# Kernel tuning notes

Measured on AMD Instinct MI355X. Metric: run time of the kernel, lower is better.

## Reference

```python
import jax, jax.numpy as jnp
import numpy as np

B, S, D, H = 4, 2048, 1024, 16
DK = D // H


def setup_inputs() -> dict:
    key = jax.random.key(0)
    ks = jax.random.split(key, 10)
    s = 0.02  # keep linear outputs well-scaled
    causal = jnp.triu(jnp.ones((S, S), dtype=bool), k=1)  # True = masked
    return {
        "Q": jax.random.normal(ks[0], (B, S, D), dtype=jnp.float32),
        "K_V": jax.random.normal(ks[1], (B, S, D), dtype=jnp.float32),
        "mask": jnp.broadcast_to(causal, (B, S, S)),
        "Wq": jax.random.normal(ks[2], (D, D), dtype=jnp.float32) * s,
        "bq": jnp.zeros((D,), dtype=jnp.float32),
        "Wk": jax.random.normal(ks[3], (D, D), dtype=jnp.float32) * s,
        "bk": jnp.zeros((D,), dtype=jnp.float32),
        "Wv": jax.random.normal(ks[4], (D, D), dtype=jnp.float32) * s,
        "bv": jnp.zeros((D,), dtype=jnp.float32),
        "Wo": jax.random.normal(ks[5], (D, D), dtype=jnp.float32) * s,
        "bo": jnp.zeros((D,), dtype=jnp.float32),
    }


def reference(Q, K_V, mask, Wq, bq, Wk, bk, Wv, bv, Wo, bo):
    # Linear projections
    q = Q @ Wq + bq          # [B, Sq, D]
    k = K_V @ Wk + bk        # [B, Sk, D]
    v = K_V @ Wv + bv        # [B, Sk, D]
    Sq, Sk = q.shape[1], k.shape[1]
    # chunk(dim=2)+cat(dim=0) == split into H heads of size DK
    q = q.reshape(B, Sq, H, DK)
    k = k.reshape(B, Sk, H, DK)
    v = v.reshape(B, Sk, H, DK)
    scale = 1.0 / jnp.sqrt(jnp.float32(DK))
    scores = jnp.einsum("bqhd,bkhd->bhqk", q, k) * scale  # [B,H,Sq,Sk]
    # mask.repeat(head_num,1,1) == broadcast mask over heads
    scores = jnp.where(mask[:, None, :, :], -jnp.inf, scores)
    attn = jax.nn.softmax(scores, axis=-1)
    # dropout is identity in eval mode
    out = jnp.einsum("bhqk,bkhd->bqhd", attn, v).reshape(B, Sq, D)
    return out @ Wo + bo
```

## Files before the change

### kernel.cpp

```cpp
#include <hip/hip_runtime.h>

typedef unsigned short u16;
typedef __attribute__((ext_vector_type(8))) __bf16 bf16x8;
typedef __attribute__((ext_vector_type(4))) float f32x4;

#define B_  4
#define S_  2048
#define D_  1024
#define H_  16
#define DK_ 64

__device__ __forceinline__ u16 f2bf(float f) {
  unsigned u = __float_as_uint(f);
  u += 0x7fffu + ((u >> 16) & 1u);
  return (u16)(u >> 16);
}
__device__ __forceinline__ u16 f2bf_trunc(float f) {
  return (u16)(__float_as_uint(f) >> 16);
}
__device__ __forceinline__ float hexp2(float f) {
  return __builtin_amdgcn_exp2f(f);
}

__device__ __forceinline__ void load_lds16(const u16* g, u16* l) {
  __builtin_amdgcn_global_load_lds((const __attribute__((address_space(1))) void*)g,
                                   (__attribute__((address_space(3))) void*)l,
                                   16, 0, 0);
}

__global__ void cvt_bf16_2(const float* __restrict__ x0, u16* __restrict__ y0,
                           const float* __restrict__ x1, u16* __restrict__ y1, int n4) {
  int i = blockIdx.x * blockDim.x + threadIdx.x;
  const float* x = x0; u16* y = y0;
  int j = i;
  if (i >= n4) { x = x1; y = y1; j = i - n4; }
  float4 v = ((const float4*)x)[j];
  ushort4 o;
  o.x = f2bf(v.x); o.y = f2bf(v.y); o.z = f2bf(v.z); o.w = f2bf(v.w);
  ((ushort4*)y)[j] = o;
}

__global__ void transpose_cvt4(const float* __restrict__ W0, const float* __restrict__ W1,
                               const float* __restrict__ W2, const float* __restrict__ W3,
                               u16* __restrict__ T0, u16* __restrict__ T1,
                               u16* __restrict__ T2, u16* __restrict__ T3) {
  __shared__ float tile[32][33];
  const float* W = (blockIdx.z == 0) ? W0 : (blockIdx.z == 1) ? W1 : (blockIdx.z == 2) ? W2 : W3;
  u16*         T = (blockIdx.z == 0) ? T0 : (blockIdx.z == 1) ? T1 : (blockIdx.z == 2) ? T2 : T3;
  int bx = blockIdx.x * 32, by = blockIdx.y * 32;
  int tx = threadIdx.x, ty = threadIdx.y;
  #pragma unroll
  for (int i = 0; i < 32; i += 8)
    tile[ty + i][tx] = W[(size_t)(by + ty + i) * D_ + bx + tx];
  __syncthreads();
  #pragma unroll
  for (int i = 0; i < 32; i += 8)
    T[(size_t)(bx + ty + i) * D_ + by + tx] = f2bf(tile[tx][ty + i]);
}

#define BM 128
#define BN 128
#define BK 32

__global__ __launch_bounds__(256, 2)
void gemm_qkv(const u16* __restrict__ Aq, const u16* __restrict__ Ak,
              const u16* __restrict__ Bt3,
              const float* __restrict__ bq, const float* __restrict__ bk,
              const float* __restrict__ bv,
              u16* __restrict__ qp, u16* __restrict__ kp, u16* __restrict__ vpT,
              float qscale) {
  __shared__ u16 As[BM * BK];
  __shared__ u16 Bs[BN * BK];
  const int tid  = threadIdx.x;
  const int lane = tid & 63, wave = tid >> 6;
  const int bm = blockIdx.x * BM;
  const int bn = blockIdx.y * BN;
  const int path = bn >> 10;
  const u16* A = (path == 0) ? Aq : Ak;
  const int wm = (wave >> 1) * 64, wn = (wave & 1) * 64;
  const int fm = lane & 15, fk4 = lane >> 4;
  const int K = D_;

  f32x4 acc[4][4] = {};

  const int r = tid >> 2;
  const int c = (tid & 3) * 8;
  const u16* gA0 = A   + (size_t)(bm + r) * K + c;
  const u16* gA1 = A   + (size_t)(bm + r + 64) * K + c;
  const u16* gB0 = Bt3 + (size_t)(bn + r) * K + c;
  const u16* gB1 = Bt3 + (size_t)(bn + r + 64) * K + c;
  u16* lA0 = &As[tid * 8];
  u16* lA1 = &As[2048 + tid * 8];
  u16* lB0 = &Bs[tid * 8];
  u16* lB1 = &Bs[2048 + tid * 8];

  for (int kt = 0; kt < K; kt += BK) {
    load_lds16(gA0 + kt, lA0);
    load_lds16(gA1 + kt, lA1);
    load_lds16(gB0 + kt, lB0);
    load_lds16(gB1 + kt, lB1);
    __syncthreads();
    bf16x8 af[4], bfr[4];
    #pragma unroll
    for (int i = 0; i < 4; ++i)
      af[i] = *(const bf16x8*)&As[(wm + i * 16 + fm) * BK + fk4 * 8];
    #pragma unroll
    for (int i = 0; i < 4; ++i)
      bfr[i] = *(const bf16x8*)&Bs[(wn + i * 16 + fm) * BK + fk4 * 8];
    #pragma unroll
    for (int i = 0; i < 4; ++i)
      #pragma unroll
      for (int j = 0; j < 4; ++j)
        acc[i][j] = __builtin_amdgcn_mfma_f32_16x16x32_bf16(af[i], bfr[j], acc[i][j], 0, 0, 0);
    __syncthreads();
  }

  #pragma unroll
  for (int i = 0; i < 4; ++i) {
    #pragma unroll
    for (int j = 0; j < 4; ++j) {
      int colg = bn + wn + j * 16 + fm;
      int rowg0 = bm + wm + i * 16 + fk4 * 4;
      if (path == 0) {
        float bb = bq[colg];
        #pragma unroll
        for (int rg = 0; rg < 4; ++rg)
          qp[(size_t)(rowg0 + rg) * D_ + colg] = f2bf((acc[i][j][rg] + bb) * qscale);
      } else if (path == 1) {
        int ck = colg - 1024;
        float bb = bk[ck];
        #pragma unroll
        for (int rg = 0; rg < 4; ++rg)
          kp[(size_t)(rowg0 + rg) * D_ + ck] = f2bf(acc[i][j][rg] + bb);
      } else {
        int cv = colg - 2048;
        float bb = bv[cv];
        int hh = cv >> 6, dk = cv & 63;
        int bbt = rowg0 >> 11, s = rowg0 & (S_ - 1);
        ushort4 pk4;
        pk4.x = f2bf(acc[i][j][0] + bb);
        pk4.y = f2bf(acc[i][j][1] + bb);
        pk4.z = f2bf(acc[i][j][2] + bb);
        pk4.w = f2bf(acc[i][j][3] + bb);
        *(ushort4*)&vpT[(((size_t)bbt * H_ + hh) * DK_ + dk) * S_ + s] = pk4;
      }
    }
  }
}

__global__ __launch_bounds__(256, 2)
void gemm_out(const u16* __restrict__ A, const u16* __restrict__ Bt,
              const float* __restrict__ bias, float* __restrict__ Cf) {
  __shared__ u16 As[BM * BK];
  __shared__ u16 Bs[BN * BK];
  const int tid  = threadIdx.x;
  const int lane = tid & 63, wave = tid >> 6;
  const int bm = blockIdx.x * BM;
  const int bn = blockIdx.y * BN;
  const int wm = (wave >> 1) * 64, wn = (wave & 1) * 64;
  const int fm = lane & 15, fk4 = lane >> 4;
  const int K = D_;

  f32x4 acc[4][4] = {};
  const int r = tid >> 2;
  const int c = (tid & 3) * 8;
  const u16* gA0 = A  + (size_t)(bm + r) * K + c;
  const u16* gA1 = A  + (size_t)(bm + r + 64) * K + c;
  const u16* gB0 = Bt + (size_t)(bn + r) * K + c;
  const u16* gB1 = Bt + (size_t)(bn + r + 64) * K + c;
  u16* lA0 = &As[tid * 8];
  u16* lA1 = &As[2048 + tid * 8];
  u16* lB0 = &Bs[tid * 8];
  u16* lB1 = &Bs[2048 + tid * 8];

  for (int kt = 0; kt < K; kt += BK) {
    load_lds16(gA0 + kt, lA0);
    load_lds16(gA1 + kt, lA1);
    load_lds16(gB0 + kt, lB0);
    load_lds16(gB1 + kt, lB1);
    __syncthreads();
    bf16x8 af[4], bfr[4];
    #pragma unroll
    for (int i = 0; i < 4; ++i)
      af[i] = *(const bf16x8*)&As[(wm + i * 16 + fm) * BK + fk4 * 8];
    #pragma unroll
    for (int i = 0; i < 4; ++i)
      bfr[i] = *(const bf16x8*)&Bs[(wn + i * 16 + fm) * BK + fk4 * 8];
    #pragma unroll
    for (int i = 0; i < 4; ++i)
      #pragma unroll
      for (int j = 0; j < 4; ++j)
        acc[i][j] = __builtin_amdgcn_mfma_f32_16x16x32_bf16(af[i], bfr[j], acc[i][j], 0, 0, 0);
    __syncthreads();
  }

  #pragma unroll
  for (int i = 0; i < 4; ++i)
    #pragma unroll
    for (int j = 0; j < 4; ++j) {
      int colg = bn + wn + j * 16 + fm;
      float bb = bias[colg];
      #pragma unroll
      for (int rg = 0; rg < 4; ++rg) {
        int rowg = bm + wm + i * 16 + fk4 * 4 + rg;
        Cf[(size_t)rowg * D_ + colg] = acc[i][j][rg] + bb;
      }
    }
}

#define PST 136

__global__ __launch_bounds__(256, 2)
void attn_kernel(const u16* __restrict__ qp, const u16* __restrict__ kp,
                 const u16* __restrict__ vpT, u16* __restrict__ ao) {
  __shared__ u16 Ks[16 * 512];
  __shared__ u16 Vs[16 * 512];
  __shared__ u16 Ps[4 * 32 * PST];

  const int tid  = threadIdx.x;
  const int lane = tid & 63;
  const int w    = tid >> 6;
  const int fm   = lane & 15;
  const int fk4  = lane >> 4;

  const int i = blockIdx.x;
  const int b = i & 3;
  const int h = (i >> 2) & 15;
  const int p = i >> 6;

  u16* Pw = &Ps[w * 32 * PST];
  const u16* kb = kp  + (size_t)(b * S_) * D_ + h * DK_;
  const u16* vb = vpT + (size_t)((b * H_ + h) * DK_) * S_;

  #pragma unroll 1
  for (int sidx = 0; sidx < 2; ++sidx) {
    const int qt = (sidx == 0) ? p : 15 - p;
    const int q0 = qt * 128 + w * 32;
    const int nj = qt + 1;

    bf16x8 aq[2][2];
    #pragma unroll
    for (int qf = 0; qf < 2; ++qf)
      #pragma unroll
      for (int kh = 0; kh < 2; ++kh)
        aq[qf][kh] = *(const bf16x8*)(qp + (size_t)(b * S_ + q0 + qf * 16 + fm) * D_
                                         + h * DK_ + kh * 32 + fk4 * 8);

    f32x4 oacc[2][4] = {};
    float l0 = 0.f, l1 = 0.f;

    #pragma unroll 1
    for (int j = 0; j < nj; ++j) {
      const int kv0 = j * 128;
      const bool lastt = (j == qt);

      __syncthreads();
      #pragma unroll
      for (int c = 0; c < 4; ++c) {
        int idx = 4 * w + c;
        load_lds16(kb + (size_t)(kv0 + (idx >> 1) * 16 + fm) * D_ + (idx & 1) * 32 + fk4 * 8,
                   &Ks[idx * 512 + lane * 8]);
      }
      #pragma unroll
      for (int c = 0; c < 4; ++c) {
        int idx = 4 * w + c;
        load_lds16(vb + (size_t)((idx & 3) * 16 + fm) * S_ + kv0 + (idx >> 2) * 32 + fk4 * 8,
                   &Vs[idx * 512 + lane * 8]);
      }
      __syncthreads();

      #pragma unroll
      for (int mt = 0; mt < 8; ++mt) {
        bf16x8 kf0 = *(const bf16x8*)&Ks[(mt * 2 + 0) * 512 + lane * 8];
        bf16x8 kf1 = *(const bf16x8*)&Ks[(mt * 2 + 1) * 512 + lane * 8];
        f32x4 z0 = {0.f, 0.f, 0.f, 0.f}, z1 = z0;
        z0 = __builtin_amdgcn_mfma_f32_16x16x32_bf16(kf0, aq[0][0], z0, 0, 0, 0);
        z0 = __builtin_amdgcn_mfma_f32_16x16x32_bf16(kf1, aq[0][1], z0, 0, 0, 0);
        z1 = __builtin_amdgcn_mfma_f32_16x16x32_bf16(kf0, aq[1][0], z1, 0, 0, 0);
        z1 = __builtin_amdgcn_mfma_f32_16x16x32_bf16(kf1, aq[1][1], z1, 0, 0, 0);

        const int kvr = kv0 + mt * 16 + fk4 * 4;
        ushort4 p0, p1;
        #pragma unroll
        for (int rg = 0; rg < 4; ++rg) {
          float zz0 = z0[rg], zz1 = z1[rg];
          if (lastt) {
            if (kvr + rg > q0 + fm)      zz0 = -1e30f;
            if (kvr + rg > q0 + 16 + fm) zz1 = -1e30f;
          }
          float e0 = hexp2(zz0);
          float e1 = hexp2(zz1);
          l0 += e0; l1 += e1;
          ((u16*)&p0)[rg] = f2bf_trunc(e0);
          ((u16*)&p1)[rg] = f2bf_trunc(e1);
        }
        *(ushort4*)&Pw[(fm)      * PST + mt * 16 + fk4 * 4] = p0;
        *(ushort4*)&Pw[(16 + fm) * PST + mt * 16 + fk4 * 4] = p1;
      }

      #pragma unroll
      for (int kt = 0; kt < 4; ++kt) {
        bf16x8 ap0 = *(const bf16x8*)&Pw[(fm)      * PST + kt * 32 + fk4 * 8];
        bf16x8 ap1 = *(const bf16x8*)&Pw[(16 + fm) * PST + kt * 32 + fk4 * 8];
        #pragma unroll
        for (int nt = 0; nt < 4; ++nt) {
          bf16x8 bv = *(const bf16x8*)&Vs[(kt * 4 + nt) * 512 + lane * 8];
          oacc[0][nt] = __builtin_amdgcn_mfma_f32_16x16x32_bf16(ap0, bv, oacc[0][nt], 0, 0, 0);
          oacc[1][nt] = __builtin_amdgcn_mfma_f32_16x16x32_bf16(ap1, bv, oacc[1][nt], 0, 0, 0);
        }
      }
    }

    #pragma unroll
    for (int qf = 0; qf < 2; ++qf) {
      float ls = (qf == 0) ? l0 : l1;
      ls += __shfl_xor(ls, 16, 64);
      ls += __shfl_xor(ls, 32, 64);
      #pragma unroll
      for (int rg = 0; rg < 4; ++rg) {
        float lr = __shfl(ls, fk4 * 4 + rg, 64);
        float inv = 1.0f / lr;
        int q = q0 + qf * 16 + fk4 * 4 + rg;
        #pragma unroll
        for (int nt = 0; nt < 4; ++nt) {
          float o = oacc[qf][nt][rg] * inv;
          ao[(size_t)(b * S_ + q) * D_ + h * DK_ + nt * 16 + fm] = f2bf(o);
        }
      }
    }
  }
}

extern "C" void kernel_launch(void* const* d_in, const int* in_sizes, int n_in,
                              void* d_out, int out_size, void* d_ws, size_t ws_size,
                              hipStream_t stream) {
  const float* Q  = (const float*)d_in[0];
  const float* KV = (const float*)d_in[1];
  const float* Wq = (const float*)d_in[3];
  const float* bq = (const float*)d_in[4];
  const float* Wk = (const float*)d_in[5];
  const float* bk = (const float*)d_in[6];
  const float* Wv = (const float*)d_in[7];
  const float* bv = (const float*)d_in[8];
  const float* Wo = (const float*)d_in[9];
  const float* bo = (const float*)d_in[10];
  float* out = (float*)d_out;

  char* ws = (char*)d_ws;
  u16* Qb  = (u16*)(ws);
  u16* Kb  = (u16*)(ws + (16ull << 20));
  u16* Wqt = (u16*)(ws + (32ull << 20));
  u16* Wkt = (u16*)(ws + (34ull << 20));
  u16* Wvt = (u16*)(ws + (36ull << 20));
  u16* Wot = (u16*)(ws + (38ull << 20));
  u16* qp  = (u16*)(ws + (40ull << 20));
  u16* kp  = (u16*)(ws + (56ull << 20));
  u16* vpT = (u16*)(ws + (72ull << 20));
  u16* ao  = Qb;

  const int n4 = (B_ * S_ * D_) / 4;
  cvt_bf16_2<<<2 * n4 / 256, 256, 0, stream>>>(Q, Qb, KV, Kb, n4);

  transpose_cvt4<<<dim3(32, 32, 4), dim3(32, 8), 0, stream>>>(Wq, Wk, Wv, Wo,
                                                              Wqt, Wkt, Wvt, Wot);

  const float qscale = 0.125f * 1.44269504f;
  gemm_qkv<<<dim3(64, 24), 256, 0, stream>>>(Qb, Kb, Wqt, bq, bk, bv,
                                             qp, kp, vpT, qscale);

  attn_kernel<<<512, 256, 0, stream>>>(qp, kp, vpT, ao);

  gemm_out<<<dim3(64, 8), 256, 0, stream>>>(ao, Wot, bo, out);
}
```

Before: 325.4 us.

## Replace projection GEMMs with 8-wave triple-buffered swizzled-LDS pipelined GEMM

Both projection GEMMs are replaced by one templated kernel with 256x128x64 tiles, 512 threads and a three-stage LDS ring. Global-to-LDS loads for tile t+2 are issued while tile t is computed, using explicit vmcnt waits and barriers, and the LDS layout is XOR-swizzled to avoid bank conflicts. MFMA sections are raised in priority with setprio. The goal is to hide global memory latency and raise MFMA utilisation. The cost is a large LDS footprint, which may limit occupancy, and fewer blocks per GEMM.

After: 327.8 us. About the same (+0.7%).

```diff
diff --git a/kernel.cpp b/kernel.cpp
--- a/kernel.cpp
+++ b/kernel.cpp
@@ -58,154 +58,145 @@
     T[(size_t)(bx + ty + i) * D_ + by + tx] = f2bf(tile[tx][ty + i]);
 }
 
-#define BM 128
-#define BN 128
-#define BK 32
-
-__global__ __launch_bounds__(256, 2)
-void gemm_qkv(const u16* __restrict__ Aq, const u16* __restrict__ Ak,
-              const u16* __restrict__ Bt3,
-              const float* __restrict__ bq, const float* __restrict__ bk,
-              const float* __restrict__ bv,
-              u16* __restrict__ qp, u16* __restrict__ kp, u16* __restrict__ vpT,
-              float qscale) {
-  __shared__ u16 As[BM * BK];
-  __shared__ u16 Bs[BN * BK];
+#define GBM 256
+#define GBN 128
+#define GBK 64
+#define ABUF 16384
+#define BBUF 8192
+#define TBUF 24576
+#define NT_  (D_ / GBK)
+
+template<int MODE>
+__global__ __launch_bounds__(512, 2)
+void gemm8p(const u16* __restrict__ Aq, const u16* __restrict__ Ak,
+            const u16* __restrict__ Bt,
+            const float* __restrict__ bq, const float* __restrict__ bk,
+            const float* __restrict__ bv,
+            u16* __restrict__ qp, u16* __restrict__ kp, u16* __restrict__ vpT,
+            float* __restrict__ Cf, float qscale) {
+  __shared__ __align__(16) u16 sm[3 * TBUF];
   const int tid  = threadIdx.x;
   const int lane = tid & 63, wave = tid >> 6;
-  const int bm = blockIdx.x * BM;
-  const int bn = blockIdx.y * BN;
-  const int path = bn >> 10;
-  const u16* A = (path == 0) ? Aq : Ak;
+  const int bm = blockIdx.x * GBM;
+  const int bn = blockIdx.y * GBN;
   const int wm = (wave >> 1) * 64, wn = (wave & 1) * 64;
   const int fm = lane & 15, fk4 = lane >> 4;
   const int K = D_;
 
+  int path = 0;
+  const u16* A = Aq;
+  if constexpr (MODE == 0) { path = bn >> 10; if (path != 0) A = Ak; }
+
+  const int srow = tid >> 3;
+  const int scol = ((tid & 7) ^ (srow & 7)) * 8;
+  const u16* gA = A  + (size_t)(bm + srow) * K + scol;
+  const u16* gB = Bt + (size_t)(bn + srow) * K + scol;
+
+#define STAGE_A(c, t, l) load_lds16(gA + (size_t)((l) * 64) * K + (t) * GBK, \
+                                    &sm[(c) * TBUF + ((l) * 512 + tid) * 8])
+#define STAGE_B(c, t, l) load_lds16(gB + (size_t)((l) * 64) * K + (t) * GBK, \
+                                    &sm[(c) * TBUF + ABUF + ((l) * 512 + tid) * 8])
+
+#define AIDX(c, rl, ks) ((c) * TBUF + (rl) * 64 + ((((ks) * 32) + fk4 * 8) ^ (((rl) & 7) << 3)))
+#define BIDX(c, rl, ks) ((c) * TBUF + ABUF + (rl) * 64 + ((((ks) * 32) + fk4 * 8) ^ (((rl) & 7) << 3)))
+
   f32x4 acc[4][4] = {};
 
-  const int r = tid >> 2;
-  const int c = (tid & 3) * 8;
-  const u16* gA0 = A   + (size_t)(bm + r) * K + c;
-  const u16* gA1 = A   + (size_t)(bm + r + 64) * K + c;
-  const u16* gB0 = Bt3 + (size_t)(bn + r) * K + c;
-  const u16* gB1 = Bt3 + (size_t)(bn + r + 64) * K + c;
-  u16* lA0 = &As[tid * 8];
-  u16* lA1 = &As[2048 + tid * 8];
-  u16* lB0 = &Bs[tid * 8];
-  u16* lB1 = &Bs[2048 + tid * 8];
-
-  for (int kt = 0; kt < K; kt += BK) {
-    load_lds16(gA0 + kt, lA0);
-    load_lds16(gA1 + kt, lA1);
-    load_lds16(gB0 + kt, lB0);
-    load_lds16(gB1 + kt, lB1);
-    __syncthreads();
-    bf16x8 af[4], bfr[4];
-    #pragma unroll
-    for (int i = 0; i < 4; ++i)
-      af[i] = *(const bf16x8*)&As[(wm + i * 16 + fm) * BK + fk4 * 8];
-    #pragma unroll
-    for (int i = 0; i < 4; ++i)
-      bfr[i] = *(const bf16x8*)&Bs[(wn + i * 16 + fm) * BK + fk4 * 8];
-    #pragma unroll
-    for (int i = 0; i < 4; ++i)
+  STAGE_A(0, 0, 0); STAGE_A(0, 0, 1); STAGE_A(0, 0, 2); STAGE_A(0, 0, 3);
+  STAGE_B(0, 0, 0); STAGE_B(0, 0, 1);
+  asm volatile("" ::: "memory");
+  STAGE_A(1, 1, 0); STAGE_A(1, 1, 1); STAGE_A(1, 1, 2); STAGE_A(1, 1, 3);
+  STAGE_B(1, 1, 0); STAGE_B(1, 1, 1);
+
+  #pragma unroll
+  for (int t = 0; t < NT_; ++t) {
+    const int cb = t % 3;
+    const int pc = (t + 2) % 3;
+    const bool pf = (t + 2) < NT_;
+    if (t + 1 < NT_) asm volatile("s_waitcnt vmcnt(6)" ::: "memory");
+    else             asm volatile("s_waitcnt vmcnt(0)" ::: "memory");
+    __builtin_amdgcn_s_barrier();
+
+    #pragma unroll
+    for (int mh = 0; mh < 2; ++mh) {
+      if (mh == 0) {
+        if (pf) { STAGE_A(pc, t + 2, 0); STAGE_A(pc, t + 2, 1); STAGE_A(pc, t + 2, 2); }
+      } else {
+        if (pf) { STAGE_A(pc, t + 2, 3); STAGE_B(pc, t + 2, 0); STAGE_B(pc, t + 2, 1); }
+      }
+      bf16x8 af[2][2], bfr[4][2];
+      #pragma unroll
+      for (int ii = 0; ii < 2; ++ii)
+        #pragma unroll
+        for (int ks = 0; ks < 2; ++ks)
+          af[ii][ks] = *(const bf16x8*)&sm[AIDX(cb, wm + (mh * 2 + ii) * 16 + fm, ks)];
       #pragma unroll
       for (int j = 0; j < 4; ++j)
-        acc[i][j] = __builtin_amdgcn_mfma_f32_16x16x32_bf16(af[i], bfr[j], acc[i][j], 0, 0, 0);
-    __syncthreads();
-  }
-
-  #pragma unroll
-  for (int i = 0; i < 4; ++i) {
-    #pragma unroll
-    for (int j = 0; j < 4; ++j) {
-      int colg = bn + wn + j * 16 + fm;
-      int rowg0 = bm + wm + i * 16 + fk4 * 4;
-      if (path == 0) {
-        float bb = bq[colg];
-        #pragma unroll
-        for (int rg = 0; rg < 4; ++rg)
-          qp[(size_t)(rowg0 + rg) * D_ + colg] = f2bf((acc[i][j][rg] + bb) * qscale);
-      } else if (path == 1) {
-        int ck = colg - 1024;
-        float bb = bk[ck];
-        #pragma unroll
-        for (int rg = 0; rg < 4; ++rg)
-          kp[(size_t)(rowg0 + rg) * D_ + ck] = f2bf(acc[i][j][rg] + bb);
-      } else {
-        int cv = colg - 2048;
-        float bb = bv[cv];
-        int hh = cv >> 6, dk = cv & 63;
-        int bbt = rowg0 >> 11, s = rowg0 & (S_ - 1);
-        ushort4 pk4;
-        pk4.x = f2bf(acc[i][j][0] + bb);
-        pk4.y = f2bf(acc[i][j][1] + bb);
-        pk4.z = f2bf(acc[i][j][2] + bb);
-        pk4.w = f2bf(acc[i][j][3] + bb);
-        *(ushort4*)&vpT[(((size_t)bbt * H_ + hh) * DK_ + dk) * S_ + s] = pk4;
-      }
+        #pragma unroll
+        for (int ks = 0; ks < 2; ++ks)
+          bfr[j][ks] = *(const bf16x8*)&sm[BIDX(cb, wn + j * 16 + fm, ks)];
+      __builtin_amdgcn_s_barrier();
+      asm volatile("s_waitcnt lgkmcnt(0)" ::: "memory");
+      __builtin_amdgcn_s_setprio(1);
+      #pragma unroll
+      for (int ks = 0; ks < 2; ++ks)
+        #pragma unroll
+        for (int ii = 0; ii < 2; ++ii)
+          #pragma unroll
+          for (int j = 0; j < 4; ++j)
+            acc[mh * 2 + ii][j] = __builtin_amdgcn_mfma_f32_16x16x32_bf16(
+                af[ii][ks], bfr[j][ks], acc[mh * 2 + ii][j], 0, 0, 0);
+      __builtin_amdgcn_s_setprio(0);
+      __builtin_amdgcn_s_barrier();
     }
   }
-}
-
-__global__ __launch_bounds__(256, 2)
-void gemm_out(const u16* __restrict__ A, const u16* __restrict__ Bt,
-              const float* __restrict__ bias, float* __restrict__ Cf) {
-  __shared__ u16 As[BM * BK];
-  __shared__ u16 Bs[BN * BK];
-  const int tid  = threadIdx.x;
-  const int lane = tid & 63, wave = tid >> 6;
-  const int bm = blockIdx.x * BM;
-  const int bn = blockIdx.y * BN;
-  const int wm = (wave >> 1) * 64, wn = (wave & 1) * 64;
-  const int fm = lane & 15, fk4 = lane >> 4;
-  const int K = D_;
-
-  f32x4 acc[4][4] = {};
-  const int r = tid >> 2;
-  const int c = (tid & 3) * 8;
-  const u16* gA0 = A  + (size_t)(bm + r) * K + c;
-  const u16* gA1 = A  + (size_t)(bm + r + 64) * K + c;
-  const u16* gB0 = Bt + (size_t)(bn + r) * K + c;
-  const u16* gB1 = Bt + (size_t)(bn + r + 64) * K + c;
-  u16* lA0 = &As[tid * 8];
-  u16* lA1 = &As[2048 + tid * 8];
-  u16* lB0 = &Bs[tid * 8];
-  u16* lB1 = &Bs[2048 + tid * 8];
-
-  for (int kt = 0; kt < K; kt += BK) {
-    load_lds16(gA0 + kt, lA0);
-    load_lds16(gA1 + kt, lA1);
-    load_lds16(gB0 + kt, lB0);
-    load_lds16(gB1 + kt, lB1);
-    __syncthreads();
-    bf16x8 af[4], bfr[4];
+
+  if constexpr (MODE == 0) {
+    #pragma unroll
+    for (int i = 0; i < 4; ++i) {
+      #pragma unroll
+      for (int j = 0; j < 4; ++j) {
+        int colg = bn + wn + j * 16 + fm;
+        int rowg0 = bm + wm + i * 16 + fk4 * 4;
+        if (path == 0) {
+          float bb = bq[colg];
+          #pragma unroll
+          for (int rg = 0; rg < 4; ++rg)
+            qp[(size_t)(rowg0 + rg) * D_ + colg] = f2bf((acc[i][j][rg] + bb) * qscale);
+        } else if (path == 1) {
+          int ck = colg - 1024;
+          float bb = bk[ck];
+          #pragma unroll
+          for (int rg = 0; rg < 4; ++rg)
+            kp[(size_t)(rowg0 + rg) * D_ + ck] = f2bf(acc[i][j][rg] + bb);
+        } else {
+          int cv = colg - 2048;
+          float bb = bv[cv];
+          int hh = cv >> 6, dk = cv & 63;
+          int bbt = rowg0 >> 11, s = rowg0 & (S_ - 1);
+          ushort4 pk4;
+          pk4.x = f2bf(acc[i][j][0] + bb);
+          pk4.y = f2bf(acc[i][j][1] + bb);
+          pk4.z = f2bf(acc[i][j][2] + bb);
+          pk4.w = f2bf(acc[i][j][3] + bb);
+          *(ushort4*)&vpT[(((size_t)bbt * H_ + hh) * DK_ + dk) * S_ + s] = pk4;
+        }
+      }
+    }
+  } else {
     #pragma unroll
     for (int i = 0; i < 4; ++i)
-      af[i] = *(const bf16x8*)&As[(wm + i * 16 + fm) * BK + fk4 * 8];
-    #pragma unroll
-    for (int i = 0; i < 4; ++i)
-      bfr[i] = *(const bf16x8*)&Bs[(wn + i * 16 + fm) * BK + fk4 * 8];
-    #pragma unroll
-    for (int i = 0; i < 4; ++i)
-      #pragma unroll
-      for (int j = 0; j < 4; ++j)
-        acc[i][j] = __builtin_amdgcn_mfma_f32_16x16x32_bf16(af[i], bfr[j], acc[i][j], 0, 0, 0);
-    __syncthreads();
+      #pragma unroll
+      for (int j = 0; j < 4; ++j) {
+        int colg = bn + wn + j * 16 + fm;
+        float bb = bq[colg];
+        #pragma unroll
+        for (int rg = 0; rg < 4; ++rg) {
+          int rowg = bm + wm + i * 16 + fk4 * 4 + rg;
+          Cf[(size_t)rowg * D_ + colg] = acc[i][j][rg] + bb;
+        }
+      }
   }
-
-  #pragma unroll
-  for (int i = 0; i < 4; ++i)
-    #pragma unroll
-    for (int j = 0; j < 4; ++j) {
-      int colg = bn + wn + j * 16 + fm;
-      float bb = bias[colg];
-      #pragma unroll
-      for (int rg = 0; rg < 4; ++rg) {
-        int rowg = bm + wm + i * 16 + fk4 * 4 + rg;
-        Cf[(size_t)rowg * D_ + colg] = acc[i][j][rg] + bb;
-      }
-    }
 }
 
 #define PST 136
@@ -365,10 +356,11 @@
                                                               Wqt, Wkt, Wvt, Wot);
 
   const float qscale = 0.125f * 1.44269504f;
-  gemm_qkv<<<dim3(64, 24), 256, 0, stream>>>(Qb, Kb, Wqt, bq, bk, bv,
-                                             qp, kp, vpT, qscale);
+  gemm8p<0><<<dim3(8192 / GBM, 3072 / GBN), 512, 0, stream>>>(
+      Qb, Kb, Wqt, bq, bk, bv, qp, kp, vpT, nullptr, qscale);
 
   attn_kernel<<<512, 256, 0, stream>>>(qp, kp, vpT, ao);
 
-  gemm_out<<<dim3(64, 8), 256, 0, stream>>>(ao, Wot, bo, out);
-}
+  gemm8p<1><<<dim3(8192 / GBM, 1024 / GBN), 512, 0, stream>>>(
+      ao, nullptr, Wot, bo, nullptr, nullptr, nullptr, nullptr, nullptr, out, 1.0f);
+}
```
